# Performance work log

Measured on AMD Instinct MI355X. Metric: run time of the kernel, lower is better.

Reference implementation:

```python
import jax, jax.numpy as jnp
import numpy as np

K = 15      # key_points
DZ = 64     # depth_bins
LD_XY = 0.01  # heatmap_2d.LocationMap loc_delta (uniform grid: loc = index * delta)
LD_Z = 0.1    # heatmap_1d.LocationMap loc_delta
LIMB = jnp.array([0, 0, 1, 1, 1, 3, 4, 5, 6, 2, 2, 9, 10, 11, 12], dtype=jnp.int32)
SYM = jnp.array([0, 1, 2, 4, 3, 6, 5, 8, 7, 10, 9, 12, 11, 14, 13], dtype=jnp.int32)


def setup_inputs() -> dict:
    key = jax.random.key(0)
    k1, k2 = jax.random.split(key)
    feature = jax.random.normal(k1, (32, 192, 192, K + DZ), dtype=jnp.float32)
    gt_kp = jax.random.uniform(k2, (32, K, 3), dtype=jnp.float32)
    return {"feature": feature, "gt_kp": gt_kp}


def reference(feature, gt_kp):
    B, H, W, _ = feature.shape
    dt = feature.dtype

    # ---- KeypointBatchToGT (vectorized; replaces TensorArray loops) ----
    max_loc = (jnp.array([H, W], dtype=dt) - 1.0) * LD_XY
    max_z = LD_Z * (DZ - 1)
    gt_xy = jnp.minimum(gt_kp[:, :, 0:2], max_loc)                      # [B,K,2]
    ix = jnp.clip(jnp.round(gt_xy[..., 0] / LD_XY).astype(jnp.int32), 0, H - 1)  # [B,K]
    iy = jnp.clip(jnp.round(gt_xy[..., 1] / LD_XY).astype(jnp.int32), 0, W - 1)
    bidx = jnp.broadcast_to(jnp.arange(B)[:, None], (B, K))
    gt_loc_z = jnp.minimum(gt_kp[:, :, 2], max_z)                        # [B,K]

    # ---- xy branch (vectorized over keypoints; softmax over H*W) ----
    f_xy = feature[..., :K].reshape(B, H * W, K)
    p_xy = jax.nn.softmax(f_xy, axis=1).reshape(B, H, W, K)
    lm = jnp.stack(jnp.meshgrid(jnp.arange(H, dtype=dt),
                                jnp.arange(W, dtype=dt), indexing='ij'), -1) * LD_XY  # [H,W,2]
    loc_xy = jnp.einsum('bhwk,hwc->bkc', p_xy, lm)                       # [B,K,2] = E[loc]
    # variance: E[||m||^2] - ||E[m]||^2 (avoids materializing [B,H,W,K,2])
    m2 = jnp.sum(lm * lm, axis=-1)                                       # [H,W]
    var_xy = jnp.einsum('bhwk,hw->bk', p_xy, m2) - jnp.sum(loc_xy ** 2, -1)
    loss_xy = jnp.sum((loc_xy - gt_xy) ** 2, axis=-1) + var_xy           # [B,K]

    # ---- z branch (softmax over depth bins, masked/scattered at gt xy indices) ----
    p_z = jax.nn.softmax(feature[..., K:], axis=-1)                      # [B,H,W,DZ]
    mask = jnp.zeros((B, H, W), dt).at[bidx, ix, iy].set(1.0)            # mask_from_index
    p_m = p_z * mask[..., None]                                          # mask_propability_map
    gt_z_map = jnp.zeros((B, H, W), dt).at[bidx, ix, iy].set(gt_loc_z)   # expand_gt
    lz = jnp.arange(DZ, dtype=dt) * LD_Z                                 # 1d loc map
    loc_z = p_m @ lz                                                     # [B,H,W]
    var_z = p_m @ (lz * lz) - loc_z ** 2
    loss_z_map = (loc_z - gt_z_map) ** 2 + var_z                         # [B,H,W]
    loss_z = loss_z_map[bidx, ix, iy]                                    # gather_nd -> [B,K]
    loc_z_point = loc_z[bidx, ix, iy][..., None]                         # [B,K,1]

    # ---- hard-keypoint reweighting ----
    def hard(l):
        s = (jnp.sum(l) + 0.001) / K
        lb = jnp.sum(l, axis=0)          # [K]
        return lb * (lb / s)

    loss = jnp.sum(hard(loss_xy) + hard(loss_z))

    # limb / symmetry terms are computed in the original but NOT added to the
    # returned loss; reproduced here (cheap, DCE'd under jit):
    loc_xyz = jnp.concatenate([loc_xy, loc_z_point], axis=-1)            # [B,K,3]
    limbs = jnp.linalg.norm(loc_xyz - loc_xyz[:, LIMB], axis=-1, keepdims=True)
    _sym = jnp.sum((limbs - limbs[:, SYM]) ** 2)

    return loss
```

## Files before the change

### kernel.cpp

```cpp
#include <hip/hip_runtime.h>
#include <math.h>

#define K_KP 15
#define DZB  64
#define HH   192
#define WW   192
#define CH   79
#define BATCH 32
#define HWPIX (HH*WW)
#define GROUPS_PER_BATCH (HWPIX/4)
#define NGROUPS (BATCH*GROUPS_PER_BATCH)
#define BLKA 256
#define NBLKA (NGROUPS/BLKA)
#define BLOCKS_PER_BATCH (GROUPS_PER_BATCH/BLKA)

__global__ __launch_bounds__(BLKA) void kA(const float* __restrict__ feat,
                                           float* __restrict__ partials) {
  const int tid = threadIdx.x;
  const int g   = blockIdx.x * BLKA + tid;
  const int gg  = g % GROUPS_PER_BATCH;
  const int row = gg / 48;
  const int w0  = (gg - row * 48) * 4;
  const float hx = (float)row * 0.01f;

  const float4* __restrict__ F = (const float4*)feat;
  const size_t base = (size_t)g * 79;

  float aS[15], aW[15], aW2[15];
#pragma unroll
  for (int i = 0; i < 15; i++) { aS[i] = 0.f; aW[i] = 0.f; aW2[i] = 0.f; }

  float4 v0=F[base+0],  v1=F[base+1],  v2=F[base+2],  v3=F[base+3];
  float4 u0=F[base+19], u1=F[base+20], u2=F[base+21], u3=F[base+22], u4=F[base+23];
  float4 x0=F[base+39], x1=F[base+40], x2=F[base+41], x3=F[base+42], x4=F[base+43];
  float4 y0=F[base+59], y1=F[base+60], y2=F[base+61], y3=F[base+62];

  float wx, e, t;
#define ACC(c, val) { e = __expf(val); aS[c] += e; t = e * wx; aW[c] += t; aW2[c] += t * wx; }
  wx = (float)w0 * 0.01f;
  ACC(0,v0.x) ACC(1,v0.y) ACC(2,v0.z) ACC(3,v0.w)
  ACC(4,v1.x) ACC(5,v1.y) ACC(6,v1.z) ACC(7,v1.w)
  ACC(8,v2.x) ACC(9,v2.y) ACC(10,v2.z) ACC(11,v2.w)
  ACC(12,v3.x) ACC(13,v3.y) ACC(14,v3.z)
  wx = (float)(w0+1) * 0.01f;
  ACC(0,u0.w)
  ACC(1,u1.x) ACC(2,u1.y) ACC(3,u1.z) ACC(4,u1.w)
  ACC(5,u2.x) ACC(6,u2.y) ACC(7,u2.z) ACC(8,u2.w)
  ACC(9,u3.x) ACC(10,u3.y) ACC(11,u3.z) ACC(12,u3.w)
  ACC(13,u4.x) ACC(14,u4.y)
  wx = (float)(w0+2) * 0.01f;
  ACC(0,x0.z) ACC(1,x0.w)
  ACC(2,x1.x) ACC(3,x1.y) ACC(4,x1.z) ACC(5,x1.w)
  ACC(6,x2.x) ACC(7,x2.y) ACC(8,x2.z) ACC(9,x2.w)
  ACC(10,x3.x) ACC(11,x3.y) ACC(12,x3.z) ACC(13,x3.w)
  ACC(14,x4.x)
  wx = (float)(w0+3) * 0.01f;
  ACC(0,y0.y) ACC(1,y0.z) ACC(2,y0.w)
  ACC(3,y1.x) ACC(4,y1.y) ACC(5,y1.z) ACC(6,y1.w)
  ACC(7,y2.x) ACC(8,y2.y) ACC(9,y2.z) ACC(10,y2.w)
  ACC(11,y3.x) ACC(12,y3.y) ACC(13,y3.z) ACC(14,y3.w)
#undef ACC

  const float hx2 = hx * hx;

  __shared__ float red[30][BLKA + 1];
  __shared__ float red2[30][8];

#pragma unroll
  for (int chunk = 0; chunk < 2; ++chunk) {
    __syncthreads();
#pragma unroll
    for (int j = 0; j < 30; j++) {
      const int J = chunk * 30 + j;
      const int k = J >> 2, s = J & 3;
      float v = (s == 0) ? aS[k]
              : (s == 1) ? hx * aS[k]
              : (s == 2) ? aW[k]
                         : fmaf(hx2, aS[k], aW2[k]);
      red[j][tid] = v;
    }
    __syncthreads();
    if (tid < 240) {
      const int r = tid >> 3, sg = tid & 7;
      float a = 0.f;
#pragma unroll
      for (int i = 0; i < 32; i++) a += red[r][sg * 32 + i];
      red2[r][sg] = a;
    }
    __syncthreads();
    if (tid < 30) {
      float a = 0.f;
#pragma unroll
      for (int i = 0; i < 8; i++) a += red2[tid][i];
      partials[blockIdx.x * 60 + chunk * 30 + tid] = a;
    }
  }
}

__global__ __launch_bounds__(512) void kB(const float* __restrict__ partials,
                                          const float* __restrict__ gt,
                                          const float* __restrict__ feat,
                                          float* __restrict__ out) {
  const int tid = threadIdx.x;
  __shared__ float Lxy[480], Lz[480], sGtz[480];
  __shared__ int   sPix[480];
  __shared__ float lbx[15], lbz[15];

  const int b = tid / 15;
  const int k = tid - b * 15;

  float locz = 0.f, varz = 0.f;
  if (tid < 480) {
    float S = 0.f, Sh = 0.f, Sw = 0.f, Sr = 0.f;
    for (int j = 0; j < BLOCKS_PER_BATCH; ++j) {
      const float* p = partials + ((size_t)(b * BLOCKS_PER_BATCH + j) * 60 + k * 4);
      S += p[0]; Sh += p[1]; Sw += p[2]; Sr += p[3];
    }
    const float lx = Sh / S, ly = Sw / S;
    const float var = Sr / S - (lx * lx + ly * ly);

    const float maxloc = 191.0f * 0.01f;
    const float gtx = fminf(gt[(b * 15 + k) * 3 + 0], maxloc);
    const float gty = fminf(gt[(b * 15 + k) * 3 + 1], maxloc);
    const float gtz = fminf(gt[(b * 15 + k) * 3 + 2], 6.3f);

    const float dx = lx - gtx, dy = ly - gty;
    Lxy[tid] = dx * dx + dy * dy + var;

    int ix = (int)rintf(gtx / 0.01f); ix = min(max(ix, 0), HH - 1);
    int iy = (int)rintf(gty / 0.01f); iy = min(max(iy, 0), WW - 1);
    sPix[tid] = ix * WW + iy;
    sGtz[tid] = gtz;

    const float* fz = feat + (size_t)(b * HWPIX + ix * WW + iy) * CH + K_KP;
    float Sz = 0.f, S1 = 0.f, S2 = 0.f;
#pragma unroll
    for (int c = 0; c < DZB; ++c) {
      const float ez = __expf(fz[c]);
      const float lz = (float)c * 0.1f;
      Sz += ez;
      S1 += ez * lz;
      S2 += ez * lz * lz;
    }
    locz = S1 / Sz;
    varz = S2 / Sz - locz * locz;
  }
  __syncthreads();
  if (tid < 480) {
    const int pix = sPix[tid];
    float ge = sGtz[tid];
    for (int k2 = k + 1; k2 < 15; ++k2)
      if (sPix[b * 15 + k2] == pix) ge = sGtz[b * 15 + k2];
    const float d = locz - ge;
    Lz[tid] = d * d + varz;
  }
  __syncthreads();
  if (tid < 15) {
    float a = 0.f, c = 0.f;
    for (int b2 = 0; b2 < BATCH; ++b2) {
      a += Lxy[b2 * 15 + tid];
      c += Lz[b2 * 15 + tid];
    }
    lbx[tid] = a; lbz[tid] = c;
  }
  __syncthreads();
  if (tid == 0) {
    float sx = 0.f, sz = 0.f;
    for (int k2 = 0; k2 < 15; ++k2) { sx += lbx[k2]; sz += lbz[k2]; }
    sx = (sx + 0.001f) / 15.f;
    sz = (sz + 0.001f) / 15.f;
    float L = 0.f;
    for (int k2 = 0; k2 < 15; ++k2)
      L += lbx[k2] * (lbx[k2] / sx) + lbz[k2] * (lbz[k2] / sz);
    out[0] = L;
  }
}

extern "C" void kernel_launch(void* const* d_in, const int* in_sizes, int n_in,
                              void* d_out, int out_size, void* d_ws, size_t ws_size,
                              hipStream_t stream) {
  const float* feat = (const float*)d_in[0];
  const float* gt   = (const float*)d_in[1];
  float* out        = (float*)d_out;
  float* partials   = (float*)d_ws;

  hipLaunchKernelGGL(kA, dim3(NBLKA), dim3(BLKA), 0, stream, feat, partials);
  hipLaunchKernelGGL(kB, dim3(1), dim3(512), 0, stream, partials, gt, feat, out);
}
```

Before: 474.2 us.

## Stage keypoint channels into LDS via direct global-to-LDS loads

The first kernel now has each wave copy the 18 float4 segments it needs for its 64 pixel groups into a 72 KB shared buffer. It uses `global_load_lds` with lane-contiguous 16-byte requests, replacing per-thread strided float4 loads from global memory. Threads then read their values from LDS, and the same buffer is reused for the block reduction. The aim is better coalescing and fewer memory transactions for the sparse channel reads. The cost is a full vmcnt wait with no overlap and lower occupancy from the large LDS footprint. The second kernel also reads its per-block partials as float4 instead of scalars.

```diff
diff --git a/kernel.cpp b/kernel.cpp
--- a/kernel.cpp
+++ b/kernel.cpp
@@ -14,57 +14,87 @@
 #define NBLKA (NGROUPS/BLKA)
 #define BLOCKS_PER_BATCH (GROUPS_PER_BATCH/BLKA)
 
+typedef const __attribute__((address_space(1))) void* gas_t;
+typedef __attribute__((address_space(3))) void* las_t;
+
 __global__ __launch_bounds__(BLKA) void kA(const float* __restrict__ feat,
                                            float* __restrict__ partials) {
-  const int tid = threadIdx.x;
-  const int g   = blockIdx.x * BLKA + tid;
-  const int gg  = g % GROUPS_PER_BATCH;
+  __shared__ __align__(16) char smem[73728];
+  const int tid  = threadIdx.x;
+  const int lane = tid & 63;
+  const int wv   = tid >> 6;
+  const int gBlk  = blockIdx.x * BLKA;
+  const int gWave = gBlk + wv * 64;
+
+  {
+    const char* fb = (const char*)feat + (size_t)gWave * 1264;
+    char* lw = smem + wv * 18432;
+    int g = (lane >= 54) ? 3 : (lane >= 36) ? 2 : (lane >= 18) ? 1 : 0;
+    int s = lane - g * 18;
+#pragma unroll
+    for (int j = 0; j < 18; ++j) {
+      const int seg = (s < 4) ? 0 : (s < 9) ? 1 : (s < 14) ? 2 : 3;
+      const char* src = fb + (size_t)g * 1264 + (size_t)(s * 16 + seg * 240);
+      __builtin_amdgcn_global_load_lds((gas_t)src, (las_t)(lw + j * 1024), 16, 0, 0);
+      s += 10; g += 3;
+      if (s >= 18) { s -= 18; g += 1; }
+    }
+  }
+  asm volatile("s_waitcnt vmcnt(0)" ::: "memory");
+
+  const int gg  = (gBlk + tid) % GROUPS_PER_BATCH;
   const int row = gg / 48;
   const int w0  = (gg - row * 48) * 4;
   const float hx = (float)row * 0.01f;
 
-  const float4* __restrict__ F = (const float4*)feat;
-  const size_t base = (size_t)g * 79;
+  const float4* __restrict__ G = (const float4*)(smem + wv * 18432 + lane * 288);
 
   float aS[15], aW[15], aW2[15];
 #pragma unroll
   for (int i = 0; i < 15; i++) { aS[i] = 0.f; aW[i] = 0.f; aW2[i] = 0.f; }
-
-  float4 v0=F[base+0],  v1=F[base+1],  v2=F[base+2],  v3=F[base+3];
-  float4 u0=F[base+19], u1=F[base+20], u2=F[base+21], u3=F[base+22], u4=F[base+23];
-  float4 x0=F[base+39], x1=F[base+40], x2=F[base+41], x3=F[base+42], x4=F[base+43];
-  float4 y0=F[base+59], y1=F[base+60], y2=F[base+61], y3=F[base+62];
 
   float wx, e, t;
 #define ACC(c, val) { e = __expf(val); aS[c] += e; t = e * wx; aW[c] += t; aW2[c] += t * wx; }
-  wx = (float)w0 * 0.01f;
-  ACC(0,v0.x) ACC(1,v0.y) ACC(2,v0.z) ACC(3,v0.w)
-  ACC(4,v1.x) ACC(5,v1.y) ACC(6,v1.z) ACC(7,v1.w)
-  ACC(8,v2.x) ACC(9,v2.y) ACC(10,v2.z) ACC(11,v2.w)
-  ACC(12,v3.x) ACC(13,v3.y) ACC(14,v3.z)
-  wx = (float)(w0+1) * 0.01f;
-  ACC(0,u0.w)
-  ACC(1,u1.x) ACC(2,u1.y) ACC(3,u1.z) ACC(4,u1.w)
-  ACC(5,u2.x) ACC(6,u2.y) ACC(7,u2.z) ACC(8,u2.w)
-  ACC(9,u3.x) ACC(10,u3.y) ACC(11,u3.z) ACC(12,u3.w)
-  ACC(13,u4.x) ACC(14,u4.y)
-  wx = (float)(w0+2) * 0.01f;
-  ACC(0,x0.z) ACC(1,x0.w)
-  ACC(2,x1.x) ACC(3,x1.y) ACC(4,x1.z) ACC(5,x1.w)
-  ACC(6,x2.x) ACC(7,x2.y) ACC(8,x2.z) ACC(9,x2.w)
-  ACC(10,x3.x) ACC(11,x3.y) ACC(12,x3.z) ACC(13,x3.w)
-  ACC(14,x4.x)
-  wx = (float)(w0+3) * 0.01f;
-  ACC(0,y0.y) ACC(1,y0.z) ACC(2,y0.w)
-  ACC(3,y1.x) ACC(4,y1.y) ACC(5,y1.z) ACC(6,y1.w)
-  ACC(7,y2.x) ACC(8,y2.y) ACC(9,y2.z) ACC(10,y2.w)
-  ACC(11,y3.x) ACC(12,y3.y) ACC(13,y3.z) ACC(14,y3.w)
+  {
+    float4 v0 = G[0], v1 = G[1], v2 = G[2], v3 = G[3];
+    wx = (float)w0 * 0.01f;
+    ACC(0,v0.x) ACC(1,v0.y) ACC(2,v0.z) ACC(3,v0.w)
+    ACC(4,v1.x) ACC(5,v1.y) ACC(6,v1.z) ACC(7,v1.w)
+    ACC(8,v2.x) ACC(9,v2.y) ACC(10,v2.z) ACC(11,v2.w)
+    ACC(12,v3.x) ACC(13,v3.y) ACC(14,v3.z)
+  }
+  {
+    float4 u0 = G[4], u1 = G[5], u2 = G[6], u3 = G[7], u4 = G[8];
+    wx = (float)(w0+1) * 0.01f;
+    ACC(0,u0.w)
+    ACC(1,u1.x) ACC(2,u1.y) ACC(3,u1.z) ACC(4,u1.w)
+    ACC(5,u2.x) ACC(6,u2.y) ACC(7,u2.z) ACC(8,u2.w)
+    ACC(9,u3.x) ACC(10,u3.y) ACC(11,u3.z) ACC(12,u3.w)
+    ACC(13,u4.x) ACC(14,u4.y)
+  }
+  {
+    float4 x0 = G[9], x1 = G[10], x2 = G[11], x3 = G[12], x4 = G[13];
+    wx = (float)(w0+2) * 0.01f;
+    ACC(0,x0.z) ACC(1,x0.w)
+    ACC(2,x1.x) ACC(3,x1.y) ACC(4,x1.z) ACC(5,x1.w)
+    ACC(6,x2.x) ACC(7,x2.y) ACC(8,x2.z) ACC(9,x2.w)
+    ACC(10,x3.x) ACC(11,x3.y) ACC(12,x3.z) ACC(13,x3.w)
+    ACC(14,x4.x)
+  }
+  {
+    float4 y0 = G[14], y1 = G[15], y2 = G[16], y3 = G[17];
+    wx = (float)(w0+3) * 0.01f;
+    ACC(0,y0.y) ACC(1,y0.z) ACC(2,y0.w)
+    ACC(3,y1.x) ACC(4,y1.y) ACC(5,y1.z) ACC(6,y1.w)
+    ACC(7,y2.x) ACC(8,y2.y) ACC(9,y2.z) ACC(10,y2.w)
+    ACC(11,y3.x) ACC(12,y3.y) ACC(13,y3.z) ACC(14,y3.w)
+  }
 #undef ACC
 
   const float hx2 = hx * hx;
 
-  __shared__ float red[30][BLKA + 1];
-  __shared__ float red2[30][8];
+  float (*red)[BLKA + 1] = (float (*)[BLKA + 1])smem;
+  float (*red2)[8]       = (float (*)[8])(smem + 30 * (BLKA + 1) * sizeof(float));
 
 #pragma unroll
   for (int chunk = 0; chunk < 2; ++chunk) {
@@ -113,8 +143,9 @@
   if (tid < 480) {
     float S = 0.f, Sh = 0.f, Sw = 0.f, Sr = 0.f;
     for (int j = 0; j < BLOCKS_PER_BATCH; ++j) {
-      const float* p = partials + ((size_t)(b * BLOCKS_PER_BATCH + j) * 60 + k * 4);
-      S += p[0]; Sh += p[1]; Sw += p[2]; Sr += p[3];
+      const float4 p = *(const float4*)(partials +
+                        ((size_t)(b * BLOCKS_PER_BATCH + j) * 60 + k * 4));
+      S += p.x; Sh += p.y; Sw += p.z; Sr += p.w;
     }
     const float lx = Sh / S, ly = Sw / S;
     const float var = Sr / S - (lx * lx + ly * ly);
```

After: 474.3 us (median of 2 runs). Within noise of the previous version (+0.0%).
